# Optimization experiments

Measured on AMD Instinct MI355X. Metric: run time of the kernel, lower is better.

## Reference

```python
import jax, jax.numpy as jnp
import numpy as np

P = 3            # patch size
PAD = P // 2
K = 8            # candidates kept per pixel
N_ITERS = 5
T = 1.0


def _patch_cost(qpad, kpad, sy, sx, yg, xg):
    # qpad: [C,H+2P,W+2P]; kpad: [C,Hk+2P,Wk+2P]; sy,sx: [N,H,W] int -> cost [N,H,W]
    cost = jnp.zeros(sy.shape, qpad.dtype)
    for dy in range(P):
        for dx in range(P):
            qv = qpad[:, yg + dy, xg + dx]          # [C,H,W]
            kv = kpad[:, sy + dy, sx + dx]          # [C,N,H,W]
            cost = cost + jnp.sum((qv[:, None] - kv) ** 2, axis=0)
    return cost


def _topk_merge(costs, sy, sx, k):
    # keep k smallest costs along candidate axis 0 (sorted ascending)
    neg, idx = jax.lax.top_k(jnp.moveaxis(-costs, 0, -1), k)   # [H,W,k]
    take = lambda a: jnp.moveaxis(jnp.take_along_axis(jnp.moveaxis(a, 0, -1), idx, axis=-1), -1, 0)
    return -jnp.moveaxis(neg, -1, 0), take(sy), take(sx)


def _patchmatch(q, kf, key):
    # q: [C,H,W], kf: [C,Hk,Wk] -> shift maps sy, sx: [K,H,W] int
    C, H, W = q.shape
    Hk, Wk = kf.shape[1], kf.shape[2]
    qpad = jnp.pad(q, ((0, 0), (PAD, PAD), (PAD, PAD)))
    kpad = jnp.pad(kf, ((0, 0), (PAD, PAD), (PAD, PAD)))
    yg, xg = jnp.meshgrid(jnp.arange(H), jnp.arange(W), indexing="ij")
    # random init of K candidates per pixel
    sy = jax.random.randint(jax.random.fold_in(key, 10_000), (K, H, W), 0, Hk)
    sx = jax.random.randint(jax.random.fold_in(key, 10_001), (K, H, W), 0, Wk)
    cost = _patch_cost(qpad, kpad, sy, sx, yg, xg)
    cost, sy, sx = _topk_merge(cost, sy, sx, K)
    r0 = max(Hk, Wk) // 2
    for it in range(N_ITERS):
        by, bx = sy[0], sx[0]
        # parallel propagation from 4 neighbors (shift adjusted by offset)
        cy = [jnp.roll(by, 1, 1), jnp.roll(by, -1, 1),
              jnp.roll(by, 1, 0) + 1, jnp.roll(by, -1, 0) - 1]
        cx = [jnp.roll(bx, 1, 1) + 1, jnp.roll(bx, -1, 1) - 1,
              jnp.roll(bx, 1, 0), jnp.roll(bx, -1, 0)]
        # random search around current best with shrinking radius
        kit = jax.random.fold_in(key, it)
        for s in range(2):
            rad = max(1, r0 >> s)
            dy = jax.random.randint(jax.random.fold_in(kit, 2 * s), (H, W), -rad, rad + 1)
            dx = jax.random.randint(jax.random.fold_in(kit, 2 * s + 1), (H, W), -rad, rad + 1)
            cy.append(by + dy)
            cx.append(bx + dx)
        nsy = jnp.clip(jnp.stack(cy), 0, Hk - 1)
        nsx = jnp.clip(jnp.stack(cx), 0, Wk - 1)
        ncost = _patch_cost(qpad, kpad, nsy, nsx, yg, xg)
        cost, sy, sx = _topk_merge(jnp.concatenate([cost, ncost]),
                                   jnp.concatenate([sy, nsy]),
                                   jnp.concatenate([sx, nsx]), K)
    return sy, sx


def _attention_layer(qi, ki, vi, key):
    # shifts are integer constants (search is non-differentiable in original)
    sy, sx = _patchmatch(jax.lax.stop_gradient(qi), jax.lax.stop_gradient(ki), key)
    H, W = qi.shape[1], qi.shape[2]
    yg, xg = jnp.meshgrid(jnp.arange(H), jnp.arange(W), indexing="ij")
    qpad = jnp.pad(qi, ((0, 0), (PAD, PAD), (PAD, PAD)))
    kpad = jnp.pad(ki, ((0, 0), (PAD, PAD), (PAD, PAD)))
    cost = _patch_cost(qpad, kpad, sy, sx, yg, xg)       # [K,H,W]
    w = jax.nn.softmax(-cost / T, axis=0)                # [K,H,W]
    vg = vi[:, sy, sx]                                   # [Cv,K,H,W]
    return jnp.sum(w[None] * vg, axis=1)                 # [Cv,H,W]


def setup_inputs() -> dict:
    key = jax.random.key(0)
    kq, kk, kv = jax.random.split(key, 3)
    q = jax.random.normal(kq, (2, 32, 256, 256), dtype=jnp.float32)
    k = jax.random.normal(kk, (2, 32, 256, 256), dtype=jnp.float32)
    v = jax.random.normal(kv, (2, 64, 256, 256), dtype=jnp.float32)
    return {"q": q, "k": k, "v": v}


def reference(q, k, v) -> jnp.ndarray:
    B = q.shape[0]
    keys = jax.random.split(jax.random.key(42), B)
    return jax.vmap(_attention_layer)(q, k, v, keys)     # [B,Cv,H,W]
```

## Files before the change

### kernel.cpp

```cpp
#include <hip/hip_runtime.h>
#include <stdint.h>

#define HW 256
#define HWP 258
#define CH 32
#define CVN 64
#define NPIX (HW*HW)
#define KK 8
#define CSTRT (HWP*HWP)


__host__ __device__ __forceinline__ void tf2x32(uint32_t k0, uint32_t k1,
                                                uint32_t x0, uint32_t x1,
                                                uint32_t &o0, uint32_t &o1) {
  const uint32_t ks2 = k0 ^ k1 ^ 0x1BD11BDAu;
  x0 += k0; x1 += k1;
#define TFR(r) x0 += x1; x1 = (x1 << (r)) | (x1 >> (32 - (r))); x1 ^= x0;
  TFR(13) TFR(15) TFR(26) TFR(6)
  x0 += k1;  x1 += ks2 + 1u;
  TFR(17) TFR(29) TFR(16) TFR(24)
  x0 += ks2; x1 += k0 + 2u;
  TFR(13) TFR(15) TFR(26) TFR(6)
  x0 += k0;  x1 += k1 + 3u;
  TFR(17) TFR(29) TFR(16) TFR(24)
  x0 += k1;  x1 += ks2 + 4u;
  TFR(13) TFR(15) TFR(26) TFR(6)
  x0 += ks2; x1 += k0 + 5u;
#undef TFR
  o0 = x0; o1 = x1;
}

__device__ __forceinline__ uint32_t tfbits(uint32_t k0, uint32_t k1, uint32_t idx) {
  uint32_t a, b;
  tf2x32(k0, k1, 0u, idx, a, b);
  return a ^ b;
}

__global__ __launch_bounds__(256) void tpad_k(const float* __restrict__ src,
                                              float* __restrict__ dst) {
  __shared__ float tile[CH][65];
  int t = blockIdx.x;
  int b = t >> 10;
  int p0 = (t & 1023) * 64;
  int tid = threadIdx.x;
  const float* sb = src + (size_t)b * CH * NPIX;
#pragma unroll
  for (int i = 0; i < 8; i++) {
    int idx = i * 256 + tid;
    int c = idx >> 6, px = idx & 63;
    tile[c][px] = sb[c * NPIX + p0 + px];
  }
  __syncthreads();
  float* db = dst + (size_t)b * CSTRT * CH;
#pragma unroll
  for (int i = 0; i < 8; i++) {
    int idx = i * 256 + tid;
    int px = idx >> 5, c = idx & 31;
    int p = p0 + px;
    int y = p >> 8, x = p & 255;
    db[((size_t)(y + 1) * HWP + (x + 1)) * CH + c] = tile[c][px];
  }
}

__global__ __launch_bounds__(256) void vtr_k(const float* __restrict__ v,
                                             float* __restrict__ vp) {
  __shared__ float tile[CVN][65];
  int t = blockIdx.x;
  int b = t >> 10;
  int p0 = (t & 1023) * 64;
  int tid = threadIdx.x;
  const float* sb = v + (size_t)b * CVN * NPIX;
#pragma unroll
  for (int i = 0; i < 16; i++) {
    int idx = i * 256 + tid;
    int c = idx >> 6, px = idx & 63;
    tile[c][px] = sb[c * NPIX + p0 + px];
  }
  __syncthreads();
  float* db = vp + (size_t)b * NPIX * CVN;
#pragma unroll
  for (int i = 0; i < 16; i++) {
    int idx = i * 256 + tid;
    int px = idx >> 6, c = idx & 63;
    db[(size_t)(p0 + px) * CVN + c] = tile[c][px];
  }
}

__device__ __forceinline__ float cost_lds(const float* __restrict__ qt, int pl,
                                          const float* __restrict__ kb2,
                                          int sy, int sx) {
#pragma clang fp contract(off)
  float S[3][3];
#pragma unroll
  for (int dy = 0; dy < 3; dy++)
#pragma unroll
    for (int dx = 0; dx < 3; dx++) S[dy][dx] = 0.f;
  const float* kb = kb2 + ((size_t)sy * HWP + sx) * CH;
#pragma unroll 2
  for (int ch = 0; ch < CH; ch += 4) {
#pragma unroll
    for (int dy = 0; dy < 3; dy++) {
#pragma unroll
      for (int dx = 0; dx < 3; dx++) {
        int xx = pl + dx;
        const float4 qv = *(const float4*)(&qt[(dy * 66 + xx) * 32 +
                                              ((ch + 4 * (xx & 7)) & 31)]);
        const float4 kv = *(const float4*)(kb + (dy * HWP + dx) * CH + ch);
        float d;
        d = qv.x - kv.x; S[dy][dx] = S[dy][dx] + d * d;
        d = qv.y - kv.y; S[dy][dx] = S[dy][dx] + d * d;
        d = qv.z - kv.z; S[dy][dx] = S[dy][dx] + d * d;
        d = qv.w - kv.w; S[dy][dx] = S[dy][dx] + d * d;
      }
    }
  }
  float cost = 0.f;
#pragma unroll
  for (int dy = 0; dy < 3; dy++)
#pragma unroll
    for (int dx = 0; dx < 3; dx++) cost = cost + S[dy][dx];
  return cost;
}

template<int NT>
__device__ __forceinline__ void load_qtile(const float* __restrict__ qpb,
                                           float* __restrict__ qt,
                                           int y, int x0, int tid) {
  for (int i = tid; i < 3 * 66 * 8; i += NT) {
    int c4 = i & 7;
    int xx = (i >> 3) % 66;
    int dy = (i >> 3) / 66;
    float4 v = *(const float4*)(qpb + ((size_t)(y + dy) * HWP + (x0 + xx)) * CH + c4 * 4);
    *(float4*)(&qt[(dy * 66 + xx) * 32 + ((c4 * 4 + 4 * (xx & 7)) & 31)]) = v;
  }
}

__global__ __launch_bounds__(256) void init5_k(
    const float* __restrict__ qp2, const float* __restrict__ kp2,
    float* __restrict__ cO, int* __restrict__ sO,
    uint32_t kA0, uint32_t kA1, uint32_t kB0, uint32_t kB1) {
  __shared__ float qt[3 * 66 * 32];
  __shared__ uint32_t ent[512];
  __shared__ float lc[64][KK];
  __shared__ int lsv[64][KK];
  __shared__ int bcnt[8], bstart[9], boff[8];
  int tid = threadIdx.x;
  int grp = blockIdx.x;
  int b = grp >> 10;
  int gp = (grp & 1023) * 64;
  int y = gp >> 8, x0 = gp & 255;
  const float* qpb = qp2 + (size_t)b * CSTRT * CH;
  const float* kpb = kp2 + (size_t)b * CSTRT * CH;
  load_qtile<256>(qpb, qt, y, x0, tid);
  if (tid < 8) bcnt[tid] = 0;
  __syncthreads();

  uint32_t k0 = b ? kB0 : kA0, k1 = b ? kB1 : kA1;
  uint32_t f0, f1, ky0, ky1, kx0, kx1;
  tf2x32(k0, k1, 0u, 10000u, f0, f1);
  tf2x32(f0, f1, 0u, 1u, ky0, ky1);
  tf2x32(k0, k1, 0u, 10001u, f0, f1);
  tf2x32(f0, f1, 0u, 1u, kx0, kx1);

  uint32_t my[2];
  int myband[2];
#pragma unroll
  for (int e = 0; e < 2; e++) {
    int idx = tid + e * 256;
    int pl = idx & 63, j = idx >> 6;
    int p = (y << 8) | (x0 + pl);
    uint32_t cand = (uint32_t)(j * NPIX + p);
    int sy = (int)(tfbits(ky0, ky1, cand) & 255u);
    int sx = (int)(tfbits(kx0, kx1, cand) & 255u);
    my[e] = ((uint32_t)sy << 17) | ((uint32_t)sx << 9) | ((uint32_t)pl << 3) | (uint32_t)j;
    myband[e] = sy >> 5;
    atomicAdd(&bcnt[myband[e]], 1);
  }
  __syncthreads();
  if (tid == 0) {
    int s = 0;
#pragma unroll
    for (int i = 0; i < 8; i++) { bstart[i] = s; boff[i] = s; s += bcnt[i]; }
    bstart[8] = s;
  }
  __syncthreads();
#pragma unroll
  for (int e = 0; e < 2; e++) {
    int pos = atomicAdd(&boff[myband[e]], 1);
    ent[pos] = my[e];
  }
  __syncthreads();

  for (int band = 0; band < 8; band++) {
    int s = bstart[band], t = bstart[band + 1];
    for (int i = s + tid; i < t; i += 256) {
      uint32_t en = ent[i];
      int j = en & 7, pl = (en >> 3) & 63;
      int sx = (en >> 9) & 255, sy = (en >> 17) & 255;
      float c = cost_lds(qt, pl, kpb, sy, sx);
      lc[pl][j] = c;
      lsv[pl][j] = (sy << 8) | sx;
    }
    __syncthreads();
  }

  if (tid < 64) {
    int pl = tid;
    float c8[KK];
    int s8[KK];
#pragma unroll
    for (int jj = 0; jj < KK; jj++) { c8[jj] = lc[pl][jj]; s8[jj] = lsv[pl][jj]; }
#pragma unroll
    for (int ph = 0; ph < KK; ph++) {
#pragma unroll
      for (int i = (ph & 1); i + 1 < KK; i += 2) {
        if (c8[i] > c8[i + 1]) {
          float tc = c8[i]; c8[i] = c8[i + 1]; c8[i + 1] = tc;
          int ts = s8[i]; s8[i] = s8[i + 1]; s8[i + 1] = ts;
        }
      }
    }
    int p = (y << 8) | (x0 + pl);
    int base = b * KK * NPIX;
#pragma unroll
    for (int jj = 0; jj < KK; jj++) {
      cO[base + jj * NPIX + p] = c8[jj];
      sO[base + jj * NPIX + p] = s8[jj];
    }
  }
}

__device__ __forceinline__ void prop_cand(const int* __restrict__ sI, int base,
                                          int y, int x, int c, int &nsy, int &nsx) {
  int np;
  if (c == 0)      np = (y << 8) | ((x + HW - 1) & (HW - 1));
  else if (c == 1) np = (y << 8) | ((x + 1) & (HW - 1));
  else if (c == 2) np = (((y + HW - 1) & (HW - 1)) << 8) | x;
  else             np = (((y + 1) & (HW - 1)) << 8) | x;
  int sv = sI[base + np];
  if (c == 0)      { nsy = sv >> 8;       nsx = (sv & 255) + 1; }
  else if (c == 1) { nsy = sv >> 8;       nsx = (sv & 255) - 1; }
  else if (c == 2) { nsy = (sv >> 8) + 1; nsx = sv & 255; }
  else             { nsy = (sv >> 8) - 1; nsx = sv & 255; }
}

__device__ __forceinline__ void rand_cand(uint32_t kit0, uint32_t kit1, int s,
                                          uint32_t p, int by, int bx,
                                          int &nsy, int &nsx) {
  uint32_t f0, f1, h0, h1, l0, l1, hi, lo;
  tf2x32(kit0, kit1, 0u, (uint32_t)(2 * s), f0, f1);
  tf2x32(f0, f1, 0u, 0u, h0, h1);
  tf2x32(f0, f1, 0u, 1u, l0, l1);
  hi = tfbits(h0, h1, p); lo = tfbits(l0, l1, p);
  int offy = (s == 0) ? (int)(((hi % 257u) + (lo % 257u)) % 257u)
                      : (int)((((hi % 129u) * 16u) + (lo % 129u)) % 129u);
  tf2x32(kit0, kit1, 0u, (uint32_t)(2 * s + 1), f0, f1);
  tf2x32(f0, f1, 0u, 0u, h0, h1);
  tf2x32(f0, f1, 0u, 1u, l0, l1);
  hi = tfbits(h0, h1, p); lo = tfbits(l0, l1, p);
  int offx = (s == 0) ? (int)(((hi % 257u) + (lo % 257u)) % 257u)
                      : (int)((((hi % 129u) * 16u) + (lo % 129u)) % 129u);
  int rad = (s == 0) ? 128 : 64;
  nsy = by + (offy - rad);
  nsx = bx + (offx - rad);
}

__global__ __launch_bounds__(192) void iter5_k(
    const float* __restrict__ qp2, const float* __restrict__ kp2,
    const float* __restrict__ cI, const int* __restrict__ sI,
    float* __restrict__ cO, int* __restrict__ sO,
    int it, uint32_t kA0, uint32_t kA1, uint32_t kB0, uint32_t kB1) {
  __shared__ float qt[3 * 66 * 32];
  __shared__ uint32_t ent[384];
  __shared__ float lc[64][6];
  __shared__ int lsv[64][6];
  __shared__ int bcnt[8], bstart[9], boff[8];
  int tid = threadIdx.x;
  int grp = blockIdx.x;
  int b = grp >> 10;
  int gp = (grp & 1023) * 64;
  int y = gp >> 8, x0 = gp & 255;
  int base = b * KK * NPIX;
  const float* qpb = qp2 + (size_t)b * CSTRT * CH;
  const float* kpb = kp2 + (size_t)b * CSTRT * CH;
  load_qtile<192>(qpb, qt, y, x0, tid);
  if (tid < 8) bcnt[tid] = 0;
  __syncthreads();

  uint32_t k0 = b ? kB0 : kA0, k1 = b ? kB1 : kA1;
  uint32_t kit0, kit1;
  tf2x32(k0, k1, 0u, (uint32_t)it, kit0, kit1);

  uint32_t my[2];
  int myband[2];
#pragma unroll
  for (int e = 0; e < 2; e++) {
    int idx = tid + e * 192;
    int pl = idx & 63, j = idx >> 6;
    int x = x0 + pl;
    int p = (y << 8) | x;
    int nsy, nsx;
    if (j < 4) {
      prop_cand(sI, base, y, x, j, nsy, nsx);
    } else {
      int svc = sI[base + p];
      rand_cand(kit0, kit1, j - 4, (uint32_t)p, svc >> 8, svc & 255, nsy, nsx);
    }
    nsy = min(max(nsy, 0), HW - 1);
    nsx = min(max(nsx, 0), HW - 1);
    my[e] = ((uint32_t)nsy << 17) | ((uint32_t)nsx << 9) | ((uint32_t)pl << 3) | (uint32_t)j;
    myband[e] = nsy >> 5;
    atomicAdd(&bcnt[myband[e]], 1);
  }
  __syncthreads();
  if (tid == 0) {
    int s = 0;
#pragma unroll
    for (int i = 0; i < 8; i++) { bstart[i] = s; boff[i] = s; s += bcnt[i]; }
    bstart[8] = s;
  }
  __syncthreads();
#pragma unroll
  for (int e = 0; e < 2; e++) {
    int pos = atomicAdd(&boff[myband[e]], 1);
    ent[pos] = my[e];
  }
  __syncthreads();

  for (int band = 0; band < 8; band++) {
    int s = bstart[band], t = bstart[band + 1];
    for (int i = s + tid; i < t; i += 192) {
      uint32_t en = ent[i];
      int j = en & 7, pl = (en >> 3) & 63;
      int sx = (en >> 9) & 255, sy = (en >> 17) & 255;
      float c = cost_lds(qt, pl, kpb, sy, sx);
      lc[pl][j] = c;
      lsv[pl][j] = (sy << 8) | sx;
    }
    __syncthreads();
  }

  if (tid < 64) {
    int pl = tid;
    int p = (y << 8) | (x0 + pl);
    float c14[KK + 6];
    int s14[KK + 6];
#pragma unroll
    for (int jj = 0; jj < KK; jj++) {
      c14[jj] = cI[base + jj * NPIX + p];
      s14[jj] = sI[base + jj * NPIX + p];
    }
#pragma unroll
    for (int jj = 0; jj < 6; jj++) {
      c14[KK + jj] = lc[pl][jj];
      s14[KK + jj] = lsv[pl][jj];
    }
#pragma unroll
    for (int ph = 0; ph < 14; ph++) {
#pragma unroll
      for (int i = (ph & 1); i + 1 < 14; i += 2) {
        if (c14[i] > c14[i + 1]) {
          float tc = c14[i]; c14[i] = c14[i + 1]; c14[i + 1] = tc;
          int ts = s14[i]; s14[i] = s14[i + 1]; s14[i + 1] = ts;
        }
      }
    }
#pragma unroll
    for (int jj = 0; jj < KK; jj++) {
      cO[base + jj * NPIX + p] = c14[jj];
      sO[base + jj * NPIX + p] = s14[jj];
    }
  }
}

__global__ __launch_bounds__(256) void attn5_k(
    const float* __restrict__ vp, const float* __restrict__ cI,
    const int* __restrict__ sI, float* __restrict__ out) {
  int g = threadIdx.x >> 6;
  int pl = threadIdx.x & 63;
  int gpix = blockIdx.x * 64 + pl;
  int b = gpix >> 16, p = gpix & 0xFFFF;
  int base = b * KK * NPIX;
  float c[KK];
  int off[KK];
#pragma unroll
  for (int j = 0; j < KK; j++) {
    c[j] = cI[base + j * NPIX + p];
    off[j] = sI[base + j * NPIX + p];
  }
  float m = c[0];
  float w[KK];
  float Z = 0.f;
#pragma unroll
  for (int j = 0; j < KK; j++) { w[j] = expf(m - c[j]); Z = Z + w[j]; }
#pragma unroll
  for (int j = 0; j < KK; j++) w[j] = w[j] / Z;
  int bd[KK];
#pragma unroll
  for (int j = 0; j < KK; j++) bd[j] = off[j] >> 12;
  const float* vb = vp + (size_t)b * NPIX * CVN + g * 16;
  float acc[16];
#pragma unroll
  for (int i = 0; i < 16; i++) acc[i] = 0.f;
  for (int band = 0; band < 16; band++) {
#pragma unroll
    for (int j = 0; j < KK; j++) {
      if (bd[j] == band) {
        const float4* vr = (const float4*)(vb + (size_t)off[j] * CVN);
#pragma unroll
        for (int t = 0; t < 4; t++) {
          float4 vv = vr[t];
          acc[t * 4 + 0] = acc[t * 4 + 0] + w[j] * vv.x;
          acc[t * 4 + 1] = acc[t * 4 + 1] + w[j] * vv.y;
          acc[t * 4 + 2] = acc[t * 4 + 2] + w[j] * vv.z;
          acc[t * 4 + 3] = acc[t * 4 + 3] + w[j] * vv.w;
        }
      }
    }
  }
  float* ob = out + (size_t)b * CVN * NPIX;
#pragma unroll
  for (int i = 0; i < 16; i++) ob[(size_t)(g * 16 + i) * NPIX + p] = acc[i];
}

extern "C" void kernel_launch(void* const* d_in, const int* in_sizes, int n_in,
                              void* d_out, int out_size, void* d_ws, size_t ws_size,
                              hipStream_t stream) {
  const float* q = (const float*)d_in[0];
  const float* k = (const float*)d_in[1];
  const float* v = (const float*)d_in[2];
  float* out = (float*)d_out;

  uint32_t kA0, kA1, kB0, kB1;
  tf2x32(0u, 42u, 0u, 0u, kA0, kA1);
  tf2x32(0u, 42u, 0u, 1u, kB0, kB1);

  const size_t szPad = (size_t)2 * CSTRT * CH;
  const size_t szCS  = (size_t)2 * KK * NPIX;
  float* qp2 = (float*)d_ws;
  float* kp2 = qp2 + szPad;
  float* cA = kp2 + szPad;
  float* cB = cA + szCS;
  int* sA = (int*)(cB + szCS);
  int* sB = sA + szCS;
  float* vp = (float*)(sB + szCS);

  hipMemsetAsync(qp2, 0, szPad * sizeof(float), stream);
  hipMemsetAsync(kp2, 0, szPad * sizeof(float), stream);
  tpad_k<<<2048, 256, 0, stream>>>(q, qp2);
  tpad_k<<<2048, 256, 0, stream>>>(k, kp2);
  vtr_k<<<2048, 256, 0, stream>>>(v, vp);

  init5_k<<<2048, 256, 0, stream>>>(qp2, kp2, cA, sA, kA0, kA1, kB0, kB1);

  float* ci = cA; int* si = sA;
  float* co = cB; int* so = sB;
  for (int it = 0; it < 5; ++it) {
    iter5_k<<<2048, 192, 0, stream>>>(qp2, kp2, ci, si, co, so, it,
                                      kA0, kA1, kB0, kB1);
    float* tc = ci; ci = co; co = tc;
    int* ts = si; si = so; so = ts;
  }
  attn5_k<<<2048, 256, 0, stream>>>(vp, ci, si, out);
}
```

Baseline: 1.201 ms.

## Halve grid with two-pass blocks, precompute RNG keys on host, skip duplicate candidates

Init and iteration kernels now run 1024 blocks of 256 threads, and each block handles two 64-pixel groups in sequence. Per-iteration Threefry subkeys are derived on the host and passed as uint4 arguments, which removes repeated per-thread key derivation. In the iteration kernel, propagated or random candidates that match an existing shift skip the patch-cost evaluation and reuse the stored cost. The band-by-band barrier loop is replaced by one flat loop over the sorted entries. This trades fewer barriers and less redundant compute for extra LDS state and serialised passes within a block.

```diff
diff --git a/kernel.cpp b/kernel.cpp
--- a/kernel.cpp
+++ b/kernel.cpp
@@ -8,6 +8,7 @@
 #define NPIX (HW*HW)
 #define KK 8
 #define CSTRT (HWP*HWP)
+#define NBLK 1024
 
 
 __host__ __device__ __forceinline__ void tf2x32(uint32_t k0, uint32_t k1,
@@ -122,11 +123,10 @@
   return cost;
 }
 
-template<int NT>
 __device__ __forceinline__ void load_qtile(const float* __restrict__ qpb,
                                            float* __restrict__ qt,
                                            int y, int x0, int tid) {
-  for (int i = tid; i < 3 * 66 * 8; i += NT) {
+  for (int i = tid; i < 3 * 66 * 8; i += 256) {
     int c4 = i & 7;
     int xx = (i >> 3) % 66;
     int dy = (i >> 3) / 66;
@@ -135,98 +135,92 @@
   }
 }
 
-__global__ __launch_bounds__(256) void init5_k(
+__global__ __launch_bounds__(256) void init6_k(
     const float* __restrict__ qp2, const float* __restrict__ kp2,
     float* __restrict__ cO, int* __restrict__ sO,
-    uint32_t kA0, uint32_t kA1, uint32_t kB0, uint32_t kB1) {
+    uint4 ikA, uint4 ikB) {
   __shared__ float qt[3 * 66 * 32];
   __shared__ uint32_t ent[512];
-  __shared__ float lc[64][KK];
-  __shared__ int lsv[64][KK];
+  __shared__ float lc[64][9];
+  __shared__ int pcand[64][9];
   __shared__ int bcnt[8], bstart[9], boff[8];
   int tid = threadIdx.x;
-  int grp = blockIdx.x;
-  int b = grp >> 10;
-  int gp = (grp & 1023) * 64;
-  int y = gp >> 8, x0 = gp & 255;
-  const float* qpb = qp2 + (size_t)b * CSTRT * CH;
-  const float* kpb = kp2 + (size_t)b * CSTRT * CH;
-  load_qtile<256>(qpb, qt, y, x0, tid);
-  if (tid < 8) bcnt[tid] = 0;
-  __syncthreads();
-
-  uint32_t k0 = b ? kB0 : kA0, k1 = b ? kB1 : kA1;
-  uint32_t f0, f1, ky0, ky1, kx0, kx1;
-  tf2x32(k0, k1, 0u, 10000u, f0, f1);
-  tf2x32(f0, f1, 0u, 1u, ky0, ky1);
-  tf2x32(k0, k1, 0u, 10001u, f0, f1);
-  tf2x32(f0, f1, 0u, 1u, kx0, kx1);
-
-  uint32_t my[2];
-  int myband[2];
-#pragma unroll
-  for (int e = 0; e < 2; e++) {
-    int idx = tid + e * 256;
-    int pl = idx & 63, j = idx >> 6;
-    int p = (y << 8) | (x0 + pl);
-    uint32_t cand = (uint32_t)(j * NPIX + p);
-    int sy = (int)(tfbits(ky0, ky1, cand) & 255u);
-    int sx = (int)(tfbits(kx0, kx1, cand) & 255u);
-    my[e] = ((uint32_t)sy << 17) | ((uint32_t)sx << 9) | ((uint32_t)pl << 3) | (uint32_t)j;
-    myband[e] = sy >> 5;
-    atomicAdd(&bcnt[myband[e]], 1);
-  }
-  __syncthreads();
-  if (tid == 0) {
-    int s = 0;
-#pragma unroll
-    for (int i = 0; i < 8; i++) { bstart[i] = s; boff[i] = s; s += bcnt[i]; }
-    bstart[8] = s;
-  }
-  __syncthreads();
-#pragma unroll
-  for (int e = 0; e < 2; e++) {
-    int pos = atomicAdd(&boff[myband[e]], 1);
-    ent[pos] = my[e];
-  }
-  __syncthreads();
-
-  for (int band = 0; band < 8; band++) {
-    int s = bstart[band], t = bstart[band + 1];
-    for (int i = s + tid; i < t; i += 256) {
-      uint32_t en = ent[i];
+  for (int pass = 0; pass < 2; ++pass) {
+    int grp = blockIdx.x + pass * NBLK;
+    int b = grp >> 10;
+    int gp = (grp & 1023) * 64;
+    int y = gp >> 8, x0 = gp & 255;
+    const float* qpb = qp2 + (size_t)b * CSTRT * CH;
+    const float* kpb = kp2 + (size_t)b * CSTRT * CH;
+    load_qtile(qpb, qt, y, x0, tid);
+    if (tid < 8) bcnt[tid] = 0;
+    __syncthreads();
+
+    uint4 K = b ? ikB : ikA;
+    uint32_t mypk[2];
+    int myband[2];
+#pragma unroll
+    for (int e2 = 0; e2 < 2; e2++) {
+      int e = tid + e2 * 256;
+      int pl = e & 63, j = e >> 6;
+      int p = (y << 8) | (x0 + pl);
+      uint32_t cand = (uint32_t)(j * NPIX + p);
+      int sy = (int)(tfbits(K.x, K.y, cand) & 255u);
+      int sx = (int)(tfbits(K.z, K.w, cand) & 255u);
+      pcand[pl][j] = (sy << 8) | sx;
+      mypk[e2] = ((uint32_t)sy << 17) | ((uint32_t)sx << 9) | ((uint32_t)pl << 3) | (uint32_t)j;
+      myband[e2] = sy >> 5;
+      atomicAdd(&bcnt[myband[e2]], 1);
+    }
+    __syncthreads();
+    if (tid == 0) {
+      int s = 0;
+#pragma unroll
+      for (int i = 0; i < 8; i++) { bstart[i] = s; boff[i] = s; s += bcnt[i]; }
+      bstart[8] = s;
+    }
+    __syncthreads();
+#pragma unroll
+    for (int e2 = 0; e2 < 2; e2++) {
+      int pos = atomicAdd(&boff[myband[e2]], 1);
+      ent[pos] = mypk[e2];
+    }
+    __syncthreads();
+
+#pragma unroll
+    for (int ii = 0; ii < 2; ii++) {
+      uint32_t en = ent[2 * tid + ii];
       int j = en & 7, pl = (en >> 3) & 63;
       int sx = (en >> 9) & 255, sy = (en >> 17) & 255;
-      float c = cost_lds(qt, pl, kpb, sy, sx);
-      lc[pl][j] = c;
-      lsv[pl][j] = (sy << 8) | sx;
-    }
-    __syncthreads();
-  }
-
-  if (tid < 64) {
-    int pl = tid;
-    float c8[KK];
-    int s8[KK];
-#pragma unroll
-    for (int jj = 0; jj < KK; jj++) { c8[jj] = lc[pl][jj]; s8[jj] = lsv[pl][jj]; }
-#pragma unroll
-    for (int ph = 0; ph < KK; ph++) {
-#pragma unroll
-      for (int i = (ph & 1); i + 1 < KK; i += 2) {
-        if (c8[i] > c8[i + 1]) {
-          float tc = c8[i]; c8[i] = c8[i + 1]; c8[i + 1] = tc;
-          int ts = s8[i]; s8[i] = s8[i + 1]; s8[i + 1] = ts;
+      lc[pl][j] = cost_lds(qt, pl, kpb, sy, sx);
+    }
+    __syncthreads();
+
+    if (tid < 64) {
+      int pl = tid;
+      float c8[KK];
+      int s8[KK];
+#pragma unroll
+      for (int jj = 0; jj < KK; jj++) { c8[jj] = lc[pl][jj]; s8[jj] = pcand[pl][jj]; }
+#pragma unroll
+      for (int ph = 0; ph < KK; ph++) {
+#pragma unroll
+        for (int i = (ph & 1); i + 1 < KK; i += 2) {
+          if (c8[i] > c8[i + 1]) {
+            float tc = c8[i]; c8[i] = c8[i + 1]; c8[i + 1] = tc;
+            int ts = s8[i]; s8[i] = s8[i + 1]; s8[i + 1] = ts;
+          }
         }
       }
-    }
-    int p = (y << 8) | (x0 + pl);
-    int base = b * KK * NPIX;
-#pragma unroll
-    for (int jj = 0; jj < KK; jj++) {
-      cO[base + jj * NPIX + p] = c8[jj];
-      sO[base + jj * NPIX + p] = s8[jj];
-    }
+      int p = (y << 8) | (x0 + pl);
+      int base = b * KK * NPIX;
+#pragma unroll
+      for (int jj = 0; jj < KK; jj++) {
+        cO[base + jj * NPIX + p] = c8[jj];
+        sO[base + jj * NPIX + p] = s8[jj];
+      }
+    }
+    __syncthreads();
   }
 }
 
@@ -244,132 +238,137 @@
   else             { nsy = (sv >> 8) - 1; nsx = sv & 255; }
 }
 
-__device__ __forceinline__ void rand_cand(uint32_t kit0, uint32_t kit1, int s,
-                                          uint32_t p, int by, int bx,
-                                          int &nsy, int &nsx) {
-  uint32_t f0, f1, h0, h1, l0, l1, hi, lo;
-  tf2x32(kit0, kit1, 0u, (uint32_t)(2 * s), f0, f1);
-  tf2x32(f0, f1, 0u, 0u, h0, h1);
-  tf2x32(f0, f1, 0u, 1u, l0, l1);
-  hi = tfbits(h0, h1, p); lo = tfbits(l0, l1, p);
-  int offy = (s == 0) ? (int)(((hi % 257u) + (lo % 257u)) % 257u)
-                      : (int)((((hi % 129u) * 16u) + (lo % 129u)) % 129u);
-  tf2x32(kit0, kit1, 0u, (uint32_t)(2 * s + 1), f0, f1);
-  tf2x32(f0, f1, 0u, 0u, h0, h1);
-  tf2x32(f0, f1, 0u, 1u, l0, l1);
-  hi = tfbits(h0, h1, p); lo = tfbits(l0, l1, p);
-  int offx = (s == 0) ? (int)(((hi % 257u) + (lo % 257u)) % 257u)
-                      : (int)((((hi % 129u) * 16u) + (lo % 129u)) % 129u);
-  int rad = (s == 0) ? 128 : 64;
-  nsy = by + (offy - rad);
-  nsx = bx + (offx - rad);
-}
-
-__global__ __launch_bounds__(192) void iter5_k(
+__device__ __forceinline__ int rand_off(uint4 K, uint32_t p, int s) {
+  uint32_t hi = tfbits(K.x, K.y, p), lo = tfbits(K.z, K.w, p);
+  return (s == 0) ? (int)(((hi % 257u) + (lo % 257u)) % 257u) - 128
+                  : (int)((((hi % 129u) * 16u) + (lo % 129u)) % 129u) - 64;
+}
+
+__global__ __launch_bounds__(256) void iter6_k(
     const float* __restrict__ qp2, const float* __restrict__ kp2,
     const float* __restrict__ cI, const int* __restrict__ sI,
     float* __restrict__ cO, int* __restrict__ sO,
-    int it, uint32_t kA0, uint32_t kA1, uint32_t kB0, uint32_t kB1) {
+    uint4 A0y, uint4 A0x, uint4 A1y, uint4 A1x,
+    uint4 B0y, uint4 B0x, uint4 B1y, uint4 B1x) {
   __shared__ float qt[3 * 66 * 32];
   __shared__ uint32_t ent[384];
-  __shared__ float lc[64][6];
-  __shared__ int lsv[64][6];
+  __shared__ float lc[64][7];
+  __shared__ int pcand[64][7];
+  __shared__ int pcur[64][9];
+  __shared__ signed char dup[64][8];
   __shared__ int bcnt[8], bstart[9], boff[8];
   int tid = threadIdx.x;
-  int grp = blockIdx.x;
-  int b = grp >> 10;
-  int gp = (grp & 1023) * 64;
-  int y = gp >> 8, x0 = gp & 255;
-  int base = b * KK * NPIX;
-  const float* qpb = qp2 + (size_t)b * CSTRT * CH;
-  const float* kpb = kp2 + (size_t)b * CSTRT * CH;
-  load_qtile<192>(qpb, qt, y, x0, tid);
-  if (tid < 8) bcnt[tid] = 0;
-  __syncthreads();
-
-  uint32_t k0 = b ? kB0 : kA0, k1 = b ? kB1 : kA1;
-  uint32_t kit0, kit1;
-  tf2x32(k0, k1, 0u, (uint32_t)it, kit0, kit1);
-
-  uint32_t my[2];
-  int myband[2];
-#pragma unroll
-  for (int e = 0; e < 2; e++) {
-    int idx = tid + e * 192;
-    int pl = idx & 63, j = idx >> 6;
-    int x = x0 + pl;
-    int p = (y << 8) | x;
-    int nsy, nsx;
-    if (j < 4) {
-      prop_cand(sI, base, y, x, j, nsy, nsx);
-    } else {
-      int svc = sI[base + p];
-      rand_cand(kit0, kit1, j - 4, (uint32_t)p, svc >> 8, svc & 255, nsy, nsx);
-    }
-    nsy = min(max(nsy, 0), HW - 1);
-    nsx = min(max(nsx, 0), HW - 1);
-    my[e] = ((uint32_t)nsy << 17) | ((uint32_t)nsx << 9) | ((uint32_t)pl << 3) | (uint32_t)j;
-    myband[e] = nsy >> 5;
-    atomicAdd(&bcnt[myband[e]], 1);
-  }
-  __syncthreads();
-  if (tid == 0) {
-    int s = 0;
-#pragma unroll
-    for (int i = 0; i < 8; i++) { bstart[i] = s; boff[i] = s; s += bcnt[i]; }
-    bstart[8] = s;
-  }
-  __syncthreads();
-#pragma unroll
-  for (int e = 0; e < 2; e++) {
-    int pos = atomicAdd(&boff[myband[e]], 1);
-    ent[pos] = my[e];
-  }
-  __syncthreads();
-
-  for (int band = 0; band < 8; band++) {
-    int s = bstart[band], t = bstart[band + 1];
-    for (int i = s + tid; i < t; i += 192) {
+  for (int pass = 0; pass < 2; ++pass) {
+    int grp = blockIdx.x + pass * NBLK;
+    int b = grp >> 10;
+    int gp = (grp & 1023) * 64;
+    int y = gp >> 8, x0 = gp & 255;
+    int base = b * KK * NPIX;
+    const float* qpb = qp2 + (size_t)b * CSTRT * CH;
+    const float* kpb = kp2 + (size_t)b * CSTRT * CH;
+    load_qtile(qpb, qt, y, x0, tid);
+    for (int e = tid; e < 512; e += 256) {
+      int pl = e & 63, jj = e >> 6;
+      pcur[pl][jj] = sI[base + jj * NPIX + ((y << 8) | (x0 + pl))];
+    }
+    if (tid < 8) bcnt[tid] = 0;
+    __syncthreads();
+
+    uint32_t mypk[2];
+    int myband[2];
+    int nown[2] = {0, 0};
+    for (int e = tid, e2 = 0; e < 384; e += 256, e2++) {
+      int pl = e & 63, j = e >> 6;
+      int x = x0 + pl;
+      int p = (y << 8) | x;
+      int nsy, nsx;
+      if (j < 4) {
+        prop_cand(sI, base, y, x, j, nsy, nsx);
+      } else {
+        int svc = pcur[pl][0];
+        int by = svc >> 8, bx = svc & 255;
+        int s = j - 4;
+        uint4 KY = b ? (s ? B1y : B0y) : (s ? A1y : A0y);
+        uint4 KX = b ? (s ? B1x : B0x) : (s ? A1x : A0x);
+        nsy = by + rand_off(KY, (uint32_t)p, s);
+        nsx = bx + rand_off(KX, (uint32_t)p, s);
+      }
+      nsy = min(max(nsy, 0), HW - 1);
+      nsx = min(max(nsx, 0), HW - 1);
+      int ps = (nsy << 8) | nsx;
+      pcand[pl][j] = ps;
+      int d = -1;
+#pragma unroll
+      for (int jj = 0; jj < KK; jj++)
+        if (d < 0 && pcur[pl][jj] == ps) d = jj;
+      dup[pl][j] = (signed char)d;
+      if (d < 0) {
+        mypk[e2] = ((uint32_t)nsy << 17) | ((uint32_t)nsx << 9) |
+                   ((uint32_t)pl << 3) | (uint32_t)j;
+        myband[e2] = nsy >> 5;
+        nown[e2] = 1;
+        atomicAdd(&bcnt[myband[e2]], 1);
+      }
+    }
+    __syncthreads();
+    if (tid == 0) {
+      int s = 0;
+#pragma unroll
+      for (int i = 0; i < 8; i++) { bstart[i] = s; boff[i] = s; s += bcnt[i]; }
+      bstart[8] = s;
+    }
+    __syncthreads();
+#pragma unroll
+    for (int e2 = 0; e2 < 2; e2++) {
+      if (nown[e2]) {
+        int pos = atomicAdd(&boff[myband[e2]], 1);
+        ent[pos] = mypk[e2];
+      }
+    }
+    __syncthreads();
+
+    int ntot = bstart[8];
+    for (int i = tid; i < ntot; i += 256) {
       uint32_t en = ent[i];
       int j = en & 7, pl = (en >> 3) & 63;
       int sx = (en >> 9) & 255, sy = (en >> 17) & 255;
-      float c = cost_lds(qt, pl, kpb, sy, sx);
-      lc[pl][j] = c;
-      lsv[pl][j] = (sy << 8) | sx;
-    }
-    __syncthreads();
-  }
-
-  if (tid < 64) {
-    int pl = tid;
-    int p = (y << 8) | (x0 + pl);
-    float c14[KK + 6];
-    int s14[KK + 6];
-#pragma unroll
-    for (int jj = 0; jj < KK; jj++) {
-      c14[jj] = cI[base + jj * NPIX + p];
-      s14[jj] = sI[base + jj * NPIX + p];
-    }
-#pragma unroll
-    for (int jj = 0; jj < 6; jj++) {
-      c14[KK + jj] = lc[pl][jj];
-      s14[KK + jj] = lsv[pl][jj];
-    }
-#pragma unroll
-    for (int ph = 0; ph < 14; ph++) {
-#pragma unroll
-      for (int i = (ph & 1); i + 1 < 14; i += 2) {
-        if (c14[i] > c14[i + 1]) {
-          float tc = c14[i]; c14[i] = c14[i + 1]; c14[i + 1] = tc;
-          int ts = s14[i]; s14[i] = s14[i + 1]; s14[i + 1] = ts;
+      lc[pl][j] = cost_lds(qt, pl, kpb, sy, sx);
+    }
+    __syncthreads();
+
+    if (tid < 64) {
+      int pl = tid;
+      int p = (y << 8) | (x0 + pl);
+      float c14[KK + 6];
+      int s14[KK + 6];
+#pragma unroll
+      for (int jj = 0; jj < KK; jj++) {
+        c14[jj] = cI[base + jj * NPIX + p];
+        s14[jj] = pcur[pl][jj];
+      }
+#pragma unroll
+      for (int j = 0; j < 6; j++) {
+        int d = dup[pl][j];
+        c14[KK + j] = (d >= 0) ? c14[d] : lc[pl][j];
+        s14[KK + j] = pcand[pl][j];
+      }
+#pragma unroll
+      for (int ph = 0; ph < 14; ph++) {
+#pragma unroll
+        for (int i = (ph & 1); i + 1 < 14; i += 2) {
+          if (c14[i] > c14[i + 1]) {
+            float tc = c14[i]; c14[i] = c14[i + 1]; c14[i + 1] = tc;
+            int ts = s14[i]; s14[i] = s14[i + 1]; s14[i + 1] = ts;
+          }
         }
       }
-    }
-#pragma unroll
-    for (int jj = 0; jj < KK; jj++) {
-      cO[base + jj * NPIX + p] = c14[jj];
-      sO[base + jj * NPIX + p] = s14[jj];
-    }
+#pragma unroll
+      for (int jj = 0; jj < KK; jj++) {
+        cO[base + jj * NPIX + p] = c14[jj];
+        sO[base + jj * NPIX + p] = s14[jj];
+      }
+    }
+    __syncthreads();
   }
 }
 
@@ -435,6 +434,15 @@
   tf2x32(0u, 42u, 0u, 0u, kA0, kA1);
   tf2x32(0u, 42u, 0u, 1u, kB0, kB1);
 
+  uint4 ikA, ikB;
+  {
+    uint32_t f0, f1;
+    tf2x32(kA0, kA1, 0u, 10000u, f0, f1); tf2x32(f0, f1, 0u, 1u, ikA.x, ikA.y);
+    tf2x32(kA0, kA1, 0u, 10001u, f0, f1); tf2x32(f0, f1, 0u, 1u, ikA.z, ikA.w);
+    tf2x32(kB0, kB1, 0u, 10000u, f0, f1); tf2x32(f0, f1, 0u, 1u, ikB.x, ikB.y);
+    tf2x32(kB0, kB1, 0u, 10001u, f0, f1); tf2x32(f0, f1, 0u, 1u, ikB.z, ikB.w);
+  }
+
   const size_t szPad = (size_t)2 * CSTRT * CH;
   const size_t szCS  = (size_t)2 * KK * NPIX;
   float* qp2 = (float*)d_ws;
@@ -451,13 +459,31 @@
   tpad_k<<<2048, 256, 0, stream>>>(k, kp2);
   vtr_k<<<2048, 256, 0, stream>>>(v, vp);
 
-  init5_k<<<2048, 256, 0, stream>>>(qp2, kp2, cA, sA, kA0, kA1, kB0, kB1);
+  init6_k<<<NBLK, 256, 0, stream>>>(qp2, kp2, cA, sA, ikA, ikB);
 
   float* ci = cA; int* si = sA;
   float* co = cB; int* so = sB;
   for (int it = 0; it < 5; ++it) {
-    iter5_k<<<2048, 192, 0, stream>>>(qp2, kp2, ci, si, co, so, it,
-                                      kA0, kA1, kB0, kB1);
+    uint4 ky[2][2], kx[2][2];
+    for (int bb = 0; bb < 2; bb++) {
+      uint32_t kk0 = bb ? kB0 : kA0, kk1 = bb ? kB1 : kA1;
+      uint32_t kit0, kit1;
+      tf2x32(kk0, kk1, 0u, (uint32_t)it, kit0, kit1);
+      for (int s = 0; s < 2; s++) {
+        uint32_t f0, f1, h0, h1, l0, l1;
+        tf2x32(kit0, kit1, 0u, (uint32_t)(2 * s), f0, f1);
+        tf2x32(f0, f1, 0u, 0u, h0, h1);
+        tf2x32(f0, f1, 0u, 1u, l0, l1);
+        ky[bb][s] = make_uint4(h0, h1, l0, l1);
+        tf2x32(kit0, kit1, 0u, (uint32_t)(2 * s + 1), f0, f1);
+        tf2x32(f0, f1, 0u, 0u, h0, h1);
+        tf2x32(f0, f1, 0u, 1u, l0, l1);
+        kx[bb][s] = make_uint4(h0, h1, l0, l1);
+      }
+    }
+    iter6_k<<<NBLK, 256, 0, stream>>>(qp2, kp2, ci, si, co, so,
+                                      ky[0][0], kx[0][0], ky[0][1], kx[0][1],
+                                      ky[1][0], kx[1][0], ky[1][1], kx[1][1]);
     float* tc = ci; ci = co; co = tc;
     int* ts = si; si = so; so = ts;
   }
```

Measured after the change: 1.536 ms. +27.8%, slower.
